# Optimization experiments

Hardware: AMD Instinct MI355X
Metric: run time of the kernel (lower is better)

The kernel has to match this reference:

```python
import jax, jax.numpy as jnp
import numpy as np

N_NODES = 100000
N_EDGES = 1600000
NUM_FEATS = 128
HIDDEN = 16
NUM_CLASSES = 40


def setup_inputs() -> dict:
    key = jax.random.key(0)
    k1, k2, k3, k4, k5 = jax.random.split(key, 5)
    x = jax.random.normal(k1, (N_NODES, NUM_FEATS), dtype=jnp.float32)
    edge_weight = jax.random.uniform(k2, (N_EDGES,), dtype=jnp.float32)
    # Glorot-uniform linear weights (bias=False in the module)
    lim1 = float(np.sqrt(6.0 / (NUM_FEATS + HIDDEN)))
    lim2 = float(np.sqrt(6.0 / (HIDDEN + NUM_CLASSES)))
    W1 = jax.random.uniform(k3, (NUM_FEATS, HIDDEN), dtype=jnp.float32, minval=-lim1, maxval=lim1)
    W2 = jax.random.uniform(k4, (HIDDEN, NUM_CLASSES), dtype=jnp.float32, minval=-lim2, maxval=lim2)
    edge_index = jax.random.randint(k5, (2, N_EDGES), 0, N_NODES, dtype=jnp.int64)
    return {"x": x, "edge_weight": edge_weight, "W1": W1, "W2": W2, "edge_index": edge_index}


def _sgconv(h, W, src, dst, edge_weight, n):
    # SGConv (K=1): weighted neighbor aggregation + self loop (weight 1), then bias-free linear
    msg = edge_weight[:, None] * h[src]                      # [E, d] gather + scale
    agg = jax.ops.segment_sum(msg, dst, num_segments=n) + h  # scatter-add + self loop
    return agg @ W


def reference(x, edge_weight, W1, W2, edge_index):
    src, dst = edge_index[0], edge_index[1]
    n = x.shape[0]
    h = _sgconv(x, W1, src, dst, edge_weight, n)   # [N, 16]
    # dropout(p=0.5) is identity in eval mode
    h = _sgconv(h, W2, src, dst, edge_weight, n)   # [N, num_classes]
    return jax.nn.log_softmax(h, axis=1)
```

## Files before the change

### kernel.cpp

```cpp
#include <hip/hip_runtime.h>

#define NFEAT 128
#define HID 16
#define NCLS 40
#define BSHIFT 7
#define BNODES 128
#define CAP 2560
#define NBUCK_MAX 800
#define BIN_CHUNK 4096
#define APAD 17
#define ZPAD 41

#define SCALE1 262144.0f
#define SCALE2 65536.0f

typedef __attribute__((ext_vector_type(8))) short short8;
typedef __attribute__((ext_vector_type(4))) float f32x4;

__device__ __forceinline__ unsigned bf16_rne(float f) {
    unsigned u = __float_as_uint(f);
    return (u + 0x7FFFu + ((u >> 16) & 1u)) >> 16;
}
__device__ __forceinline__ float bf_lo(unsigned u) { return __uint_as_float(u << 16); }
__device__ __forceinline__ float bf_hi(unsigned u) { return __uint_as_float(u & 0xFFFF0000u); }

__global__ __launch_bounds__(256) void zero_kernel(int* __restrict__ p, int m)
{
    int i = blockIdx.x * 256 + threadIdx.x;
    if (i < m) p[i] = 0;
}

__global__ __launch_bounds__(256) void bin_gemm_kernel(const int* __restrict__ src,
                                                       const int* __restrict__ dst,
                                                       const float* __restrict__ ew,
                                                       int* __restrict__ cursor,
                                                       int2* __restrict__ slab,
                                                       int E, int nbuck, int nbin,
                                                       const float* __restrict__ x,
                                                       const float* __restrict__ W1,
                                                       unsigned short* __restrict__ h1b,
                                                       int n)
{
    __shared__ int hist[NBUCK_MAX];
    __shared__ int runbase[NBUCK_MAX];
    int tid = threadIdx.x;

    if (blockIdx.x < nbin) {
        for (int i = tid; i < NBUCK_MAX; i += 256) hist[i] = 0;
        __syncthreads();

        int base = blockIdx.x * BIN_CHUNK;
        int myd[16], mys[16], myw[16];
        #pragma unroll
        for (int k = 0; k < 16; ++k) {
            int e = base + k * 256 + tid;
            if (e < E) {
                myd[k] = dst[e];
                mys[k] = src[e];
                myw[k] = __float_as_int(ew[e]);
                atomicAdd(&hist[myd[k] >> BSHIFT], 1);
            } else myd[k] = -1;
        }
        __syncthreads();
        for (int i = tid; i < nbuck; i += 256) {
            int c = hist[i];
            runbase[i] = c ? (i * CAP + atomicAdd(&cursor[i], c)) : 0;
            hist[i] = 0;
        }
        __syncthreads();
        #pragma unroll
        for (int k = 0; k < 16; ++k) {
            int d = myd[k];
            if (d >= 0) {
                int b = d >> BSHIFT;
                int pos = runbase[b] + atomicAdd(&hist[b], 1);
                if (pos < (b + 1) * CAP)
                    slab[pos] = make_int2(mys[k] | ((d & (BNODES - 1)) << 20), myw[k]);
            }
        }
    } else {
        int wave = tid >> 6, lane = tid & 63;
        int m = lane & 15, q = lane >> 4;
        int base = (blockIdx.x - nbin) * 64 + wave * 16;

        short8 bfrag[4];
        #pragma unroll
        for (int kc = 0; kc < 4; ++kc) {
            #pragma unroll
            for (int j = 0; j < 8; ++j)
                bfrag[kc][j] = (short)bf16_rne(W1[(kc * 32 + q * 8 + j) * HID + m]);
        }

        int rowa = base + m; if (rowa > n - 1) rowa = n - 1;
        const float* xr = x + (size_t)rowa * NFEAT;
        f32x4 acc = {0.f, 0.f, 0.f, 0.f};
        #pragma unroll
        for (int kc = 0; kc < 4; ++kc) {
            float4 a0 = *(const float4*)(xr + kc * 32 + q * 8);
            float4 a1 = *(const float4*)(xr + kc * 32 + q * 8 + 4);
            short8 af;
            af[0] = (short)bf16_rne(a0.x); af[1] = (short)bf16_rne(a0.y);
            af[2] = (short)bf16_rne(a0.z); af[3] = (short)bf16_rne(a0.w);
            af[4] = (short)bf16_rne(a1.x); af[5] = (short)bf16_rne(a1.y);
            af[6] = (short)bf16_rne(a1.z); af[7] = (short)bf16_rne(a1.w);
            acc = __builtin_amdgcn_mfma_f32_16x16x32_bf16(af, bfrag[kc], acc, 0, 0, 0);
        }
        #pragma unroll
        for (int reg = 0; reg < 4; ++reg) {
            int rowd = base + q * 4 + reg;
            if (rowd < n)
                h1b[(size_t)rowd * HID + m] = (unsigned short)bf16_rne(acc[reg]);
        }
    }
}

__global__ __launch_bounds__(512, 8) void gather1_kernel(const uint4* __restrict__ hq,
                                                         const int* __restrict__ cursor,
                                                         const int2* __restrict__ slab,
                                                         uint4* __restrict__ outb, int n)
{
    __shared__ int accum[BNODES * APAD];
    int tid = threadIdx.x;
    #pragma unroll
    for (int i = tid; i < BNODES * APAD; i += 512) accum[i] = 0;
    __syncthreads();

    int b = blockIdx.x;
    int beg = b * CAP;
    int cnt = cursor[b]; if (cnt > CAP) cnt = CAP;
    int total = cnt * 2;

    int i0 = tid, i1 = tid + 512, i2 = tid + 1024, i3 = tid + 1536;
    int2 e0, e1, e2, e3; uint4 q0, q1, q2;
    if (i0 < total) e0 = slab[beg + (i0 >> 1)];
    if (i1 < total) e1 = slab[beg + (i1 >> 1)];
    if (i2 < total) e2 = slab[beg + (i2 >> 1)];
    if (i3 < total) e3 = slab[beg + (i3 >> 1)];
    if (i0 < total) q0 = hq[(size_t)(e0.x & 0xFFFFF) * 2 + (i0 & 1)];
    if (i1 < total) q1 = hq[(size_t)(e1.x & 0xFFFFF) * 2 + (i1 & 1)];
    if (i2 < total) q2 = hq[(size_t)(e2.x & 0xFFFFF) * 2 + (i2 & 1)];

    while (i0 < total) {
        uint4 q3;
        if (i3 < total) q3 = hq[(size_t)(e3.x & 0xFFFFF) * 2 + (i3 & 1)];
        int i4 = i3 + 512;
        int2 e4;
        if (i4 < total) e4 = slab[beg + (i4 >> 1)];

        int p  = i0 & 1;
        int dl = (e0.x >> 20) & (BNODES - 1);
        float wsc = __int_as_float(e0.y) * SCALE1;
        int* a = &accum[dl * APAD + p * 8];
        atomicAdd(a + 0, __float2int_rn(wsc * bf_lo(q0.x)));
        atomicAdd(a + 1, __float2int_rn(wsc * bf_hi(q0.x)));
        atomicAdd(a + 2, __float2int_rn(wsc * bf_lo(q0.y)));
        atomicAdd(a + 3, __float2int_rn(wsc * bf_hi(q0.y)));
        atomicAdd(a + 4, __float2int_rn(wsc * bf_lo(q0.z)));
        atomicAdd(a + 5, __float2int_rn(wsc * bf_hi(q0.z)));
        atomicAdd(a + 6, __float2int_rn(wsc * bf_lo(q0.w)));
        atomicAdd(a + 7, __float2int_rn(wsc * bf_hi(q0.w)));

        e0 = e1; e1 = e2; e2 = e3; e3 = e4;
        q0 = q1; q1 = q2; q2 = q3;
        i0 = i1; i1 = i2; i2 = i3; i3 = i4;
    }
    __syncthreads();

    const float inv = 1.0f / SCALE1;
    if (tid < BNODES * 2) {
        int dl = tid >> 1, p = tid & 1;
        int node = (b << BSHIFT) + dl;
        if (node < n) {
            uint4 qs = hq[(size_t)node * 2 + p];
            const int* a = &accum[dl * APAD + p * 8];
            uint4 o;
            o.x = bf16_rne((float)a[0] * inv + bf_lo(qs.x)) |
                  (bf16_rne((float)a[1] * inv + bf_hi(qs.x)) << 16);
            o.y = bf16_rne((float)a[2] * inv + bf_lo(qs.y)) |
                  (bf16_rne((float)a[3] * inv + bf_hi(qs.y)) << 16);
            o.z = bf16_rne((float)a[4] * inv + bf_lo(qs.z)) |
                  (bf16_rne((float)a[5] * inv + bf_hi(qs.z)) << 16);
            o.w = bf16_rne((float)a[6] * inv + bf_lo(qs.w)) |
                  (bf16_rne((float)a[7] * inv + bf_hi(qs.w)) << 16);
            outb[(size_t)node * 2 + p] = o;
        }
    }
}

__global__ __launch_bounds__(512, 6) void gather2_lsm_kernel(const uint4* __restrict__ hq,
                                                             const int* __restrict__ cursor,
                                                             const int2* __restrict__ slab,
                                                             const float* __restrict__ W2,
                                                             float* __restrict__ out, int n)
{
    __shared__ int   accum[BNODES * APAD];
    __shared__ float w2s[HID * NCLS];
    __shared__ float zbuf[BNODES * ZPAD];
    int tid = threadIdx.x;
    #pragma unroll
    for (int i = tid; i < BNODES * APAD; i += 512) accum[i] = 0;
    for (int i = tid; i < HID * NCLS; i += 512) w2s[i] = W2[i];
    __syncthreads();

    int b = blockIdx.x;
    int beg = b * CAP;
    int cnt = cursor[b]; if (cnt > CAP) cnt = CAP;
    int node0 = b << BSHIFT;
    int total = cnt * 2;

    int i0 = tid, i1 = tid + 512, i2 = tid + 1024, i3 = tid + 1536;
    int2 e0, e1, e2, e3; uint4 q0, q1, q2;
    if (i0 < total) e0 = slab[beg + (i0 >> 1)];
    if (i1 < total) e1 = slab[beg + (i1 >> 1)];
    if (i2 < total) e2 = slab[beg + (i2 >> 1)];
    if (i3 < total) e3 = slab[beg + (i3 >> 1)];
    if (i0 < total) q0 = hq[(size_t)(e0.x & 0xFFFFF) * 2 + (i0 & 1)];
    if (i1 < total) q1 = hq[(size_t)(e1.x & 0xFFFFF) * 2 + (i1 & 1)];
    if (i2 < total) q2 = hq[(size_t)(e2.x & 0xFFFFF) * 2 + (i2 & 1)];

    while (i0 < total) {
        uint4 q3;
        if (i3 < total) q3 = hq[(size_t)(e3.x & 0xFFFFF) * 2 + (i3 & 1)];
        int i4 = i3 + 512;
        int2 e4;
        if (i4 < total) e4 = slab[beg + (i4 >> 1)];

        int p  = i0 & 1;
        int dl = (e0.x >> 20) & (BNODES - 1);
        float wsc = __int_as_float(e0.y) * SCALE2;
        int* a = &accum[dl * APAD + p * 8];
        atomicAdd(a + 0, __float2int_rn(wsc * bf_lo(q0.x)));
        atomicAdd(a + 1, __float2int_rn(wsc * bf_hi(q0.x)));
        atomicAdd(a + 2, __float2int_rn(wsc * bf_lo(q0.y)));
        atomicAdd(a + 3, __float2int_rn(wsc * bf_hi(q0.y)));
        atomicAdd(a + 4, __float2int_rn(wsc * bf_lo(q0.z)));
        atomicAdd(a + 5, __float2int_rn(wsc * bf_hi(q0.z)));
        atomicAdd(a + 6, __float2int_rn(wsc * bf_lo(q0.w)));
        atomicAdd(a + 7, __float2int_rn(wsc * bf_hi(q0.w)));

        e0 = e1; e1 = e2; e2 = e3; e3 = e4;
        q0 = q1; q1 = q2; q2 = q3;
        i0 = i1; i1 = i2; i2 = i3; i3 = i4;
    }
    __syncthreads();

    const float inv = 1.0f / SCALE2;
    if (tid < BNODES) {
        int dl = tid;
        int node = node0 + dl;
        if (node < n) {
            uint4 qa = hq[(size_t)node * 2 + 0];
            uint4 qb = hq[(size_t)node * 2 + 1];
            float r[HID];
            const int* a = &accum[dl * APAD];
            r[0]  = (float)a[ 0] * inv + bf_lo(qa.x);
            r[1]  = (float)a[ 1] * inv + bf_hi(qa.x);
            r[2]  = (float)a[ 2] * inv + bf_lo(qa.y);
            r[3]  = (float)a[ 3] * inv + bf_hi(qa.y);
            r[4]  = (float)a[ 4] * inv + bf_lo(qa.z);
            r[5]  = (float)a[ 5] * inv + bf_hi(qa.z);
            r[6]  = (float)a[ 6] * inv + bf_lo(qa.w);
            r[7]  = (float)a[ 7] * inv + bf_hi(qa.w);
            r[8]  = (float)a[ 8] * inv + bf_lo(qb.x);
            r[9]  = (float)a[ 9] * inv + bf_hi(qb.x);
            r[10] = (float)a[10] * inv + bf_lo(qb.y);
            r[11] = (float)a[11] * inv + bf_hi(qb.y);
            r[12] = (float)a[12] * inv + bf_lo(qb.z);
            r[13] = (float)a[13] * inv + bf_hi(qb.z);
            r[14] = (float)a[14] * inv + bf_lo(qb.w);
            r[15] = (float)a[15] * inv + bf_hi(qb.w);

            float z[NCLS];
            #pragma unroll
            for (int j = 0; j < NCLS; ++j) z[j] = 0.f;
            #pragma unroll
            for (int f = 0; f < HID; ++f) {
                float rf = r[f];
                #pragma unroll
                for (int j = 0; j < NCLS; ++j)
                    z[j] += rf * w2s[f * NCLS + j];
            }
            float m = z[0];
            #pragma unroll
            for (int j = 1; j < NCLS; ++j) m = fmaxf(m, z[j]);
            float ssum = 0.f;
            #pragma unroll
            for (int j = 0; j < NCLS; ++j) ssum += __expf(z[j] - m);
            float l = m + __logf(ssum);
            #pragma unroll
            for (int j = 0; j < NCLS; ++j) zbuf[dl * ZPAD + j] = z[j] - l;
        }
    }
    __syncthreads();

    for (int i = tid; i < BNODES * NCLS; i += 512) {
        int nl = i / NCLS, j = i - nl * NCLS;
        if (node0 + nl < n)
            out[(size_t)node0 * NCLS + i] = zbuf[nl * ZPAD + j];
    }
}

extern "C" void kernel_launch(void* const* d_in, const int* in_sizes, int n_in,
                              void* d_out, int out_size, void* d_ws, size_t ws_size,
                              hipStream_t stream)
{
    const float* x  = (const float*)d_in[0];
    const float* ew = (const float*)d_in[1];
    const float* W1 = (const float*)d_in[2];
    const float* W2 = (const float*)d_in[3];
    const int*   ei = (const int*)d_in[4];

    int n = in_sizes[0] / NFEAT;
    int E = in_sizes[1];
    const int* src = ei;
    const int* dst = ei + E;
    float* out = (float*)d_out;

    int nbuck = (n + BNODES - 1) >> BSHIFT;
    int nbin  = (E + BIN_CHUNK - 1) / BIN_CHUNK;
    int ngemm = (n + 63) / 64;

    char* w = (char*)d_ws;
    int*  cursor = (int*)w;  w += NBUCK_MAX * 4;
    w = (char*)(((size_t)w + 15) & ~(size_t)15);
    int2* slab   = (int2*)w; w += (size_t)NBUCK_MAX * CAP * 8;
    unsigned short* h1b = (unsigned short*)w; w += (size_t)n * HID * 2;
    unsigned short* h2b = (unsigned short*)w; w += (size_t)n * HID * 2;

    zero_kernel<<<(NBUCK_MAX + 255) / 256, 256, 0, stream>>>(cursor, NBUCK_MAX);
    bin_gemm_kernel<<<nbin + ngemm, 256, 0, stream>>>(src, dst, ew, cursor, slab,
                                                      E, nbuck, nbin, x, W1, h1b, n);
    gather1_kernel<<<nbuck, 512, 0, stream>>>((const uint4*)h1b, cursor, slab,
                                              (uint4*)h2b, n);
    gather2_lsm_kernel<<<nbuck, 512, 0, stream>>>((const uint4*)h2b, cursor, slab,
                                                  W2, out, n);
}
```

Measured before the change: 169.0 us.

## Replace bucketed LDS atomic aggregation with per-node CSR segments and register accumulation

```diff
diff --git a/kernel.cpp b/kernel.cpp
--- a/kernel.cpp
+++ b/kernel.cpp
@@ -7,12 +7,9 @@
 #define BNODES 128
 #define CAP 2560
 #define NBUCK_MAX 800
+#define NNODE_MAX 102400
 #define BIN_CHUNK 4096
-#define APAD 17
 #define ZPAD 41
-
-#define SCALE1 262144.0f
-#define SCALE2 65536.0f
 
 typedef __attribute__((ext_vector_type(8))) short short8;
 typedef __attribute__((ext_vector_type(4))) float f32x4;
@@ -30,53 +27,21 @@
     if (i < m) p[i] = 0;
 }
 
-__global__ __launch_bounds__(256) void bin_gemm_kernel(const int* __restrict__ src,
-                                                       const int* __restrict__ dst,
-                                                       const float* __restrict__ ew,
-                                                       int* __restrict__ cursor,
-                                                       int2* __restrict__ slab,
-                                                       int E, int nbuck, int nbin,
-                                                       const float* __restrict__ x,
-                                                       const float* __restrict__ W1,
-                                                       unsigned short* __restrict__ h1b,
-                                                       int n)
-{
-    __shared__ int hist[NBUCK_MAX];
-    __shared__ int runbase[NBUCK_MAX];
+__global__ __launch_bounds__(256) void count_gemm_kernel(const int* __restrict__ dst,
+                                                         int* __restrict__ deg,
+                                                         int E, int nbin,
+                                                         const float* __restrict__ x,
+                                                         const float* __restrict__ W1,
+                                                         unsigned short* __restrict__ h1b,
+                                                         int n)
+{
     int tid = threadIdx.x;
-
     if (blockIdx.x < nbin) {
-        for (int i = tid; i < NBUCK_MAX; i += 256) hist[i] = 0;
-        __syncthreads();
-
-        int base = blockIdx.x * BIN_CHUNK;
-        int myd[16], mys[16], myw[16];
+        int base = blockIdx.x * BIN_CHUNK + tid;
         #pragma unroll
         for (int k = 0; k < 16; ++k) {
-            int e = base + k * 256 + tid;
-            if (e < E) {
-                myd[k] = dst[e];
-                mys[k] = src[e];
-                myw[k] = __float_as_int(ew[e]);
-                atomicAdd(&hist[myd[k] >> BSHIFT], 1);
-            } else myd[k] = -1;
-        }
-        __syncthreads();
-        for (int i = tid; i < nbuck; i += 256) {
-            int c = hist[i];
-            runbase[i] = c ? (i * CAP + atomicAdd(&cursor[i], c)) : 0;
-            hist[i] = 0;
-        }
-        __syncthreads();
-        #pragma unroll
-        for (int k = 0; k < 16; ++k) {
-            int d = myd[k];
-            if (d >= 0) {
-                int b = d >> BSHIFT;
-                int pos = runbase[b] + atomicAdd(&hist[b], 1);
-                if (pos < (b + 1) * CAP)
-                    slab[pos] = make_int2(mys[k] | ((d & (BNODES - 1)) << 20), myw[k]);
-            }
+            int e = base + k * 256;
+            if (e < E) atomicAdd(&deg[dst[e]], 1);
         }
     } else {
         int wave = tid >> 6, lane = tid & 63;
@@ -114,186 +79,178 @@
     }
 }
 
-__global__ __launch_bounds__(512, 8) void gather1_kernel(const uint4* __restrict__ hq,
-                                                         const int* __restrict__ cursor,
-                                                         const int2* __restrict__ slab,
-                                                         uint4* __restrict__ outb, int n)
-{
-    __shared__ int accum[BNODES * APAD];
-    int tid = threadIdx.x;
+__global__ __launch_bounds__(64) void scan_kernel(const int* __restrict__ deg,
+                                                  int* __restrict__ nodebase,
+                                                  int n)
+{
+    int b = blockIdx.x, l = threadIdx.x;
+    int n0 = (b << BSHIFT) + 2 * l;
+    int d0 = (n0     < n) ? deg[n0]     : 0;
+    int d1 = (n0 + 1 < n) ? deg[n0 + 1] : 0;
+    int s = d0 + d1;
+    int incl = s;
     #pragma unroll
-    for (int i = tid; i < BNODES * APAD; i += 512) accum[i] = 0;
-    __syncthreads();
-
-    int b = blockIdx.x;
-    int beg = b * CAP;
-    int cnt = cursor[b]; if (cnt > CAP) cnt = CAP;
-    int total = cnt * 2;
-
-    int i0 = tid, i1 = tid + 512, i2 = tid + 1024, i3 = tid + 1536;
-    int2 e0, e1, e2, e3; uint4 q0, q1, q2;
-    if (i0 < total) e0 = slab[beg + (i0 >> 1)];
-    if (i1 < total) e1 = slab[beg + (i1 >> 1)];
-    if (i2 < total) e2 = slab[beg + (i2 >> 1)];
-    if (i3 < total) e3 = slab[beg + (i3 >> 1)];
-    if (i0 < total) q0 = hq[(size_t)(e0.x & 0xFFFFF) * 2 + (i0 & 1)];
-    if (i1 < total) q1 = hq[(size_t)(e1.x & 0xFFFFF) * 2 + (i1 & 1)];
-    if (i2 < total) q2 = hq[(size_t)(e2.x & 0xFFFFF) * 2 + (i2 & 1)];
-
-    while (i0 < total) {
-        uint4 q3;
-        if (i3 < total) q3 = hq[(size_t)(e3.x & 0xFFFFF) * 2 + (i3 & 1)];
-        int i4 = i3 + 512;
-        int2 e4;
-        if (i4 < total) e4 = slab[beg + (i4 >> 1)];
-
-        int p  = i0 & 1;
-        int dl = (e0.x >> 20) & (BNODES - 1);
-        float wsc = __int_as_float(e0.y) * SCALE1;
-        int* a = &accum[dl * APAD + p * 8];
-        atomicAdd(a + 0, __float2int_rn(wsc * bf_lo(q0.x)));
-        atomicAdd(a + 1, __float2int_rn(wsc * bf_hi(q0.x)));
-        atomicAdd(a + 2, __float2int_rn(wsc * bf_lo(q0.y)));
-        atomicAdd(a + 3, __float2int_rn(wsc * bf_hi(q0.y)));
-        atomicAdd(a + 4, __float2int_rn(wsc * bf_lo(q0.z)));
-        atomicAdd(a + 5, __float2int_rn(wsc * bf_hi(q0.z)));
-        atomicAdd(a + 6, __float2int_rn(wsc * bf_lo(q0.w)));
-        atomicAdd(a + 7, __float2int_rn(wsc * bf_hi(q0.w)));
-
-        e0 = e1; e1 = e2; e2 = e3; e3 = e4;
-        q0 = q1; q1 = q2; q2 = q3;
-        i0 = i1; i1 = i2; i2 = i3; i3 = i4;
-    }
-    __syncthreads();
-
-    const float inv = 1.0f / SCALE1;
-    if (tid < BNODES * 2) {
-        int dl = tid >> 1, p = tid & 1;
-        int node = (b << BSHIFT) + dl;
-        if (node < n) {
-            uint4 qs = hq[(size_t)node * 2 + p];
-            const int* a = &accum[dl * APAD + p * 8];
-            uint4 o;
-            o.x = bf16_rne((float)a[0] * inv + bf_lo(qs.x)) |
-                  (bf16_rne((float)a[1] * inv + bf_hi(qs.x)) << 16);
-            o.y = bf16_rne((float)a[2] * inv + bf_lo(qs.y)) |
-                  (bf16_rne((float)a[3] * inv + bf_hi(qs.y)) << 16);
-            o.z = bf16_rne((float)a[4] * inv + bf_lo(qs.z)) |
-                  (bf16_rne((float)a[5] * inv + bf_hi(qs.z)) << 16);
-            o.w = bf16_rne((float)a[6] * inv + bf_lo(qs.w)) |
-                  (bf16_rne((float)a[7] * inv + bf_hi(qs.w)) << 16);
-            outb[(size_t)node * 2 + p] = o;
-        }
-    }
-}
-
-__global__ __launch_bounds__(512, 6) void gather2_lsm_kernel(const uint4* __restrict__ hq,
-                                                             const int* __restrict__ cursor,
-                                                             const int2* __restrict__ slab,
-                                                             const float* __restrict__ W2,
-                                                             float* __restrict__ out, int n)
-{
-    __shared__ int   accum[BNODES * APAD];
+    for (int off = 1; off < 64; off <<= 1) {
+        int t = __shfl_up(incl, off);
+        if (l >= off) incl += t;
+    }
+    int excl = incl - s;
+    int e0 = excl;      if (e0 > CAP) e0 = CAP;
+    int e1 = excl + d0; if (e1 > CAP) e1 = CAP;
+    int base = b * CAP;
+    if (n0     < n) nodebase[n0]     = base + e0;
+    if (n0 + 1 < n) nodebase[n0 + 1] = base + e1;
+}
+
+__global__ __launch_bounds__(256) void scatter_kernel(const int* __restrict__ src,
+                                                      const int* __restrict__ dst,
+                                                      const float* __restrict__ ew,
+                                                      const int* __restrict__ nodebase,
+                                                      int* __restrict__ cursor,
+                                                      int2* __restrict__ slab, int E)
+{
+    int base = blockIdx.x * BIN_CHUNK + threadIdx.x;
+    #pragma unroll
+    for (int k = 0; k < 16; ++k) {
+        int e = base + k * 256;
+        if (e < E) {
+            int d = dst[e];
+            int pos = nodebase[d] + atomicAdd(&cursor[d], 1);
+            int bend = ((d >> BSHIFT) + 1) * CAP;
+            if (pos < bend)
+                slab[pos] = make_int2(src[e], __float_as_int(ew[e]));
+        }
+    }
+}
+
+__global__ __launch_bounds__(256) void gather1_kernel(const uint4* __restrict__ hq,
+                                                      const int* __restrict__ nodebase,
+                                                      const int* __restrict__ deg,
+                                                      const int2* __restrict__ slab,
+                                                      uint4* __restrict__ outb, int n)
+{
+    int gid = blockIdx.x * 256 + threadIdx.x;
+    int node = gid >> 1, p = gid & 1;
+    if (node >= n) return;
+
+    int beg = nodebase[node];
+    int dg  = deg[node];
+    int bend = ((node >> BSHIFT) + 1) * CAP;
+    int end = beg + dg; if (end > bend) end = bend;
+
+    uint4 own = hq[(size_t)node * 2 + p];
+    float a0 = bf_lo(own.x), a1 = bf_hi(own.x);
+    float a2 = bf_lo(own.y), a3 = bf_hi(own.y);
+    float a4 = bf_lo(own.z), a5 = bf_hi(own.z);
+    float a6 = bf_lo(own.w), a7 = bf_hi(own.w);
+
+    int k = beg;
+    int2 e0; uint4 q0;
+    if (k < end) { e0 = slab[k]; q0 = hq[(size_t)e0.x * 2 + p]; }
+    while (k < end) {
+        int kn = k + 1;
+        int2 e1; uint4 q1;
+        if (kn < end) { e1 = slab[kn]; q1 = hq[(size_t)e1.x * 2 + p]; }
+        float w = __int_as_float(e0.y);
+        a0 += w * bf_lo(q0.x); a1 += w * bf_hi(q0.x);
+        a2 += w * bf_lo(q0.y); a3 += w * bf_hi(q0.y);
+        a4 += w * bf_lo(q0.z); a5 += w * bf_hi(q0.z);
+        a6 += w * bf_lo(q0.w); a7 += w * bf_hi(q0.w);
+        e0 = e1; q0 = q1; k = kn;
+    }
+
+    uint4 o;
+    o.x = bf16_rne(a0) | (bf16_rne(a1) << 16);
+    o.y = bf16_rne(a2) | (bf16_rne(a3) << 16);
+    o.z = bf16_rne(a4) | (bf16_rne(a5) << 16);
+    o.w = bf16_rne(a6) | (bf16_rne(a7) << 16);
+    outb[(size_t)node * 2 + p] = o;
+}
+
+__global__ __launch_bounds__(256) void gather2_lsm_kernel(const uint4* __restrict__ hq,
+                                                          const int* __restrict__ nodebase,
+                                                          const int* __restrict__ deg,
+                                                          const int2* __restrict__ slab,
+                                                          const float* __restrict__ W2,
+                                                          float* __restrict__ out, int n)
+{
     __shared__ float w2s[HID * NCLS];
     __shared__ float zbuf[BNODES * ZPAD];
     int tid = threadIdx.x;
+    for (int i = tid; i < HID * NCLS; i += 256) w2s[i] = W2[i];
+
+    int node0 = blockIdx.x << BSHIFT;
+    int dl = tid >> 1, p = tid & 1;
+    int node = node0 + dl;
+    bool alive = node < n;
+
+    float a0 = 0.f, a1 = 0.f, a2 = 0.f, a3 = 0.f,
+          a4 = 0.f, a5 = 0.f, a6 = 0.f, a7 = 0.f;
+    if (alive) {
+        int beg = nodebase[node];
+        int dg  = deg[node];
+        int bend = ((node >> BSHIFT) + 1) * CAP;
+        int end = beg + dg; if (end > bend) end = bend;
+
+        uint4 own = hq[(size_t)node * 2 + p];
+        a0 = bf_lo(own.x); a1 = bf_hi(own.x);
+        a2 = bf_lo(own.y); a3 = bf_hi(own.y);
+        a4 = bf_lo(own.z); a5 = bf_hi(own.z);
+        a6 = bf_lo(own.w); a7 = bf_hi(own.w);
+
+        int k = beg;
+        int2 e0; uint4 q0;
+        if (k < end) { e0 = slab[k]; q0 = hq[(size_t)e0.x * 2 + p]; }
+        while (k < end) {
+            int kn = k + 1;
+            int2 e1; uint4 q1;
+            if (kn < end) { e1 = slab[kn]; q1 = hq[(size_t)e1.x * 2 + p]; }
+            float w = __int_as_float(e0.y);
+            a0 += w * bf_lo(q0.x); a1 += w * bf_hi(q0.x);
+            a2 += w * bf_lo(q0.y); a3 += w * bf_hi(q0.y);
+            a4 += w * bf_lo(q0.z); a5 += w * bf_hi(q0.z);
+            a6 += w * bf_lo(q0.w); a7 += w * bf_hi(q0.w);
+            e0 = e1; q0 = q1; k = kn;
+        }
+    }
+    __syncthreads();
+
+    float z[NCLS];
     #pragma unroll
-    for (int i = tid; i < BNODES * APAD; i += 512) accum[i] = 0;
-    for (int i = tid; i < HID * NCLS; i += 512) w2s[i] = W2[i];
+    for (int j = 0; j < NCLS; ++j) z[j] = 0.f;
+    if (alive) {
+        float r[8] = {a0, a1, a2, a3, a4, a5, a6, a7};
+        #pragma unroll
+        for (int f = 0; f < 8; ++f) {
+            float rf = r[f];
+            const float* wr = &w2s[(p * 8 + f) * NCLS];
+            #pragma unroll
+            for (int j = 0; j < NCLS; ++j) z[j] += rf * wr[j];
+        }
+    }
+
+    if (alive && p == 0) {
+        #pragma unroll
+        for (int j = 0; j < NCLS; ++j) zbuf[dl * ZPAD + j] = z[j];
+    }
     __syncthreads();
-
-    int b = blockIdx.x;
-    int beg = b * CAP;
-    int cnt = cursor[b]; if (cnt > CAP) cnt = CAP;
-    int node0 = b << BSHIFT;
-    int total = cnt * 2;
-
-    int i0 = tid, i1 = tid + 512, i2 = tid + 1024, i3 = tid + 1536;
-    int2 e0, e1, e2, e3; uint4 q0, q1, q2;
-    if (i0 < total) e0 = slab[beg + (i0 >> 1)];
-    if (i1 < total) e1 = slab[beg + (i1 >> 1)];
-    if (i2 < total) e2 = slab[beg + (i2 >> 1)];
-    if (i3 < total) e3 = slab[beg + (i3 >> 1)];
-    if (i0 < total) q0 = hq[(size_t)(e0.x & 0xFFFFF) * 2 + (i0 & 1)];
-    if (i1 < total) q1 = hq[(size_t)(e1.x & 0xFFFFF) * 2 + (i1 & 1)];
-    if (i2 < total) q2 = hq[(size_t)(e2.x & 0xFFFFF) * 2 + (i2 & 1)];
-
-    while (i0 < total) {
-        uint4 q3;
-        if (i3 < total) q3 = hq[(size_t)(e3.x & 0xFFFFF) * 2 + (i3 & 1)];
-        int i4 = i3 + 512;
-        int2 e4;
-        if (i4 < total) e4 = slab[beg + (i4 >> 1)];
-
-        int p  = i0 & 1;
-        int dl = (e0.x >> 20) & (BNODES - 1);
-        float wsc = __int_as_float(e0.y) * SCALE2;
-        int* a = &accum[dl * APAD + p * 8];
-        atomicAdd(a + 0, __float2int_rn(wsc * bf_lo(q0.x)));
-        atomicAdd(a + 1, __float2int_rn(wsc * bf_hi(q0.x)));
-        atomicAdd(a + 2, __float2int_rn(wsc * bf_lo(q0.y)));
-        atomicAdd(a + 3, __float2int_rn(wsc * bf_hi(q0.y)));
-        atomicAdd(a + 4, __float2int_rn(wsc * bf_lo(q0.z)));
-        atomicAdd(a + 5, __float2int_rn(wsc * bf_hi(q0.z)));
-        atomicAdd(a + 6, __float2int_rn(wsc * bf_lo(q0.w)));
-        atomicAdd(a + 7, __float2int_rn(wsc * bf_hi(q0.w)));
-
-        e0 = e1; e1 = e2; e2 = e3; e3 = e4;
-        q0 = q1; q1 = q2; q2 = q3;
-        i0 = i1; i1 = i2; i2 = i3; i3 = i4;
+    if (alive && p == 1) {
+        float zt[NCLS];
+        #pragma unroll
+        for (int j = 0; j < NCLS; ++j) zt[j] = z[j] + zbuf[dl * ZPAD + j];
+        float m = zt[0];
+        #pragma unroll
+        for (int j = 1; j < NCLS; ++j) m = fmaxf(m, zt[j]);
+        float ssum = 0.f;
+        #pragma unroll
+        for (int j = 0; j < NCLS; ++j) ssum += __expf(zt[j] - m);
+        float l = m + __logf(ssum);
+        #pragma unroll
+        for (int j = 0; j < NCLS; ++j) zbuf[dl * ZPAD + j] = zt[j] - l;
     }
     __syncthreads();
 
-    const float inv = 1.0f / SCALE2;
-    if (tid < BNODES) {
-        int dl = tid;
-        int node = node0 + dl;
-        if (node < n) {
-            uint4 qa = hq[(size_t)node * 2 + 0];
-            uint4 qb = hq[(size_t)node * 2 + 1];
-            float r[HID];
-            const int* a = &accum[dl * APAD];
-            r[0]  = (float)a[ 0] * inv + bf_lo(qa.x);
-            r[1]  = (float)a[ 1] * inv + bf_hi(qa.x);
-            r[2]  = (float)a[ 2] * inv + bf_lo(qa.y);
-            r[3]  = (float)a[ 3] * inv + bf_hi(qa.y);
-            r[4]  = (float)a[ 4] * inv + bf_lo(qa.z);
-            r[5]  = (float)a[ 5] * inv + bf_hi(qa.z);
-            r[6]  = (float)a[ 6] * inv + bf_lo(qa.w);
-            r[7]  = (float)a[ 7] * inv + bf_hi(qa.w);
-            r[8]  = (float)a[ 8] * inv + bf_lo(qb.x);
-            r[9]  = (float)a[ 9] * inv + bf_hi(qb.x);
-            r[10] = (float)a[10] * inv + bf_lo(qb.y);
-            r[11] = (float)a[11] * inv + bf_hi(qb.y);
-            r[12] = (float)a[12] * inv + bf_lo(qb.z);
-            r[13] = (float)a[13] * inv + bf_hi(qb.z);
-            r[14] = (float)a[14] * inv + bf_lo(qb.w);
-            r[15] = (float)a[15] * inv + bf_hi(qb.w);
-
-            float z[NCLS];
-            #pragma unroll
-            for (int j = 0; j < NCLS; ++j) z[j] = 0.f;
-            #pragma unroll
-            for (int f = 0; f < HID; ++f) {
-                float rf = r[f];
-                #pragma unroll
-                for (int j = 0; j < NCLS; ++j)
-                    z[j] += rf * w2s[f * NCLS + j];
-            }
-            float m = z[0];
-            #pragma unroll
-            for (int j = 1; j < NCLS; ++j) m = fmaxf(m, z[j]);
-            float ssum = 0.f;
-            #pragma unroll
-            for (int j = 0; j < NCLS; ++j) ssum += __expf(z[j] - m);
-            float l = m + __logf(ssum);
-            #pragma unroll
-            for (int j = 0; j < NCLS; ++j) zbuf[dl * ZPAD + j] = z[j] - l;
-        }
-    }
-    __syncthreads();
-
-    for (int i = tid; i < BNODES * NCLS; i += 512) {
+    for (int i = tid; i < BNODES * NCLS; i += 256) {
         int nl = i / NCLS, j = i - nl * NCLS;
         if (node0 + nl < n)
             out[(size_t)node0 * NCLS + i] = zbuf[nl * ZPAD + j];
@@ -321,17 +278,22 @@
     int ngemm = (n + 63) / 64;
 
     char* w = (char*)d_ws;
-    int*  cursor = (int*)w;  w += NBUCK_MAX * 4;
+    int* deg      = (int*)w; w += NNODE_MAX * 4;
+    int* cursor   = (int*)w; w += NNODE_MAX * 4;
+    int* nodebase = (int*)w; w += NNODE_MAX * 4;
     w = (char*)(((size_t)w + 15) & ~(size_t)15);
-    int2* slab   = (int2*)w; w += (size_t)NBUCK_MAX * CAP * 8;
+    int2* slab    = (int2*)w; w += (size_t)NBUCK_MAX * CAP * 8;
     unsigned short* h1b = (unsigned short*)w; w += (size_t)n * HID * 2;
     unsigned short* h2b = (unsigned short*)w; w += (size_t)n * HID * 2;
 
-    zero_kernel<<<(NBUCK_MAX + 255) / 256, 256, 0, stream>>>(cursor, NBUCK_MAX);
-    bin_gemm_kernel<<<nbin + ngemm, 256, 0, stream>>>(src, dst, ew, cursor, slab,
-                                                      E, nbuck, nbin, x, W1, h1b, n);
-    gather1_kernel<<<nbuck, 512, 0, stream>>>((const uint4*)h1b, cursor, slab,
-                                              (uint4*)h2b, n);
-    gather2_lsm_kernel<<<nbuck, 512, 0, stream>>>((const uint4*)h2b, cursor, slab,
-                                                  W2, out, n);
-}
+    zero_kernel<<<(2 * NNODE_MAX + 255) / 256, 256, 0, stream>>>(deg, 2 * NNODE_MAX);
+    count_gemm_kernel<<<nbin + ngemm, 256, 0, stream>>>(dst, deg, E, nbin,
+                                                        x, W1, h1b, n);
+    scan_kernel<<<nbuck, 64, 0, stream>>>(deg, nodebase, n);
+    scatter_kernel<<<nbin, 256, 0, stream>>>(src, dst, ew, nodebase, cursor, slab, E);
+    gather1_kernel<<<(2 * n + 255) / 256, 256, 0, stream>>>((const uint4*)h1b,
+                                                            nodebase, deg, slab,
+                                                            (uint4*)h2b, n);
+    gather2_lsm_kernel<<<nbuck, 256, 0, stream>>>((const uint4*)h2b, nodebase, deg,
+                                                  slab, W2, out, n);
+}
```

After: 315.8 us. 86.9% more time.
